# Performance work log

Hardware: AMD Instinct MI355X
Metric: run time of the kernel (lower is better)

The kernel has to match this reference:

```python
import jax, jax.numpy as jnp
import numpy as np

D_MODEL = 1024
D_FF = 4096
FFN_H = int(2 * D_FF / 3)  # 2730, per SwiGLUMLP
B, S = 4, 4096
LN_EPS = 1e-5
ATTN_EPS = 1e-6


def layer_norm(x, g, b):
    mu = jnp.mean(x, axis=-1, keepdims=True)
    var = jnp.mean(jnp.square(x - mu), axis=-1, keepdims=True)
    return (x - mu) * jax.lax.rsqrt(var + LN_EPS) * g + b


def setup_inputs() -> dict:
    key = jax.random.key(0)
    ks = jax.random.split(key, 16)
    s = 0.02
    return {
        "x": jax.random.normal(ks[0], (B, S, D_MODEL), dtype=jnp.float32),
        "Wqkv": jax.random.normal(ks[1], (D_MODEL, 3 * D_MODEL), dtype=jnp.float32) * s,
        "bqkv": jnp.zeros((3 * D_MODEL,), jnp.float32),
        "Wg": jax.random.normal(ks[2], (D_MODEL, FFN_H), dtype=jnp.float32) * s,
        "bg": jnp.zeros((FFN_H,), jnp.float32),
        "Wu": jax.random.normal(ks[3], (D_MODEL, FFN_H), dtype=jnp.float32) * s,
        "bu": jnp.zeros((FFN_H,), jnp.float32),
        "Wd": jax.random.normal(ks[4], (FFN_H, D_MODEL), dtype=jnp.float32) * s,
        "bd": jnp.zeros((D_MODEL,), jnp.float32),
        "g1": jnp.ones((D_MODEL,), jnp.float32),
        "b1": jnp.zeros((D_MODEL,), jnp.float32),
        "g2": jnp.ones((D_MODEL,), jnp.float32),
        "b2": jnp.zeros((D_MODEL,), jnp.float32),
    }


def reference(x, Wqkv, bqkv, Wg, bg, Wu, bu, Wd, bd, g1, b1, g2, b2):
    # QKV projection, split into q, k, v (each [B,S,D])
    qkv = jnp.einsum("bsd,de->bse", x, Wqkv) + bqkv
    q, k, v = jnp.split(qkv, 3, axis=-1)

    # Linear attention with elu(x)+1 feature map (non-causal)
    qp = jax.nn.elu(q) + 1.0
    kp = jax.nn.elu(k) + 1.0
    kv = jnp.einsum("bsd,bse->bde", kp, v)        # [B,D,D] context
    num = jnp.einsum("bsd,bde->bse", qp, kv)       # [B,S,D]
    k_sum = jnp.sum(kp, axis=1)                    # [B,D]
    den = jnp.einsum("bsd,bd->bs", qp, k_sum)[..., None]
    attn = num / (den + ATTN_EPS)

    x = layer_norm(x + attn, g1, b1)

    # SwiGLU MLP
    gate = jnp.einsum("bsd,dh->bsh", x, Wg) + bg
    up = jnp.einsum("bsd,dh->bsh", x, Wu) + bu
    ffn = jnp.einsum("bsh,hd->bsd", jax.nn.silu(gate) * up, Wd) + bd

    return layer_norm(x + ffn, g2, b2)
```

## Files before the change

kernel.cpp:

```cpp
#include <hip/hip_runtime.h>

#define SEQ 4096
#define TOK 16384
#define DM 1024
#define NQKV 3072
#define FFH 2730
#define FFHP 2816

typedef __bf16 bf16x8 __attribute__((ext_vector_type(8)));
typedef float f32x4 __attribute__((ext_vector_type(4)));

__device__ __forceinline__ unsigned short f2bf(float f) {
  union { float f; unsigned u; } v; v.f = f;
  unsigned r = v.u + 0x7fffu + ((v.u >> 16) & 1u);
  return (unsigned short)(r >> 16);
}
__device__ __forceinline__ float bf2f(unsigned short h) {
  union { unsigned u; float f; } v; v.u = ((unsigned)h) << 16;
  return v.f;
}

__device__ __forceinline__ void xcd_swizzle(int& bx, int& by) {
  const int gx = gridDim.x, gy = gridDim.y;
  const int chunk = gy >> 3;
  const int csh = __ffs(chunk) - 1;
  const int lin = by * gx + bx;
  const int xcd = lin & 7, j = lin >> 3;
  by = xcd * chunk + (j & (chunk - 1));
  bx = j >> csh;
}

enum { M_QKV = 0, M_BF16 = 1, M_NUM = 2, M_BIAS_F32 = 5 };

template<int MODE>
__global__ __launch_bounds__(256)
void gemm_kernel(const unsigned short* __restrict__ A,
                 const unsigned short* __restrict__ BT,
                 int K, int lda, int ldb, int ldc,
                 long zsA, long zsB, long zsC,
                 void* __restrict__ out0, void* __restrict__ out1, void* __restrict__ out2,
                 const float* __restrict__ bias, int nbias)
{
  __shared__ unsigned short As[2][128 * 64];
  __shared__ unsigned short Bs[2][128 * 64];
  const int tid  = threadIdx.x;
  const int wave = tid >> 6, lane = tid & 63;
  const int quad = lane >> 4, l16 = lane & 15;
  const int bz = blockIdx.z;
  int bx = blockIdx.x, by = blockIdx.y;
  xcd_swizzle(bx, by);

  const unsigned short* Ab = A + (size_t)zsA * bz + (size_t)by * 128 * lda;
  const unsigned short* Bb = BT + (size_t)zsB * bz + (size_t)bx * 128 * ldb;

  f32x4 acc[4][4] = {};

  const int srow   = lane >> 3;
  const int scol_g = (((lane & 7) ^ srow) * 8);
  const int axor   = l16 & 7;

  auto stage = [&](int buf, int k0) {
#pragma unroll
    for (int j = 0; j < 4; ++j) {
      int c = wave * 4 + j;
      const unsigned short* sa = Ab + (size_t)(c * 8 + srow) * lda + k0 + scol_g;
      __builtin_amdgcn_global_load_lds((__attribute__((address_space(1))) void*)sa,
          (__attribute__((address_space(3))) void*)(As[buf] + c * 512), 16, 0, 0);
      const unsigned short* sb = Bb + (size_t)(c * 8 + srow) * ldb + k0 + scol_g;
      __builtin_amdgcn_global_load_lds((__attribute__((address_space(1))) void*)sb,
          (__attribute__((address_space(3))) void*)(Bs[buf] + c * 512), 16, 0, 0);
    }
  };

  const int NIT = K >> 6;
  stage(0, 0);
  int cur = 0;
  for (int it = 0; it < NIT; ++it) {
    __builtin_amdgcn_s_waitcnt(0);
    __syncthreads();
    if (it + 1 < NIT) stage(cur ^ 1, (it + 1) << 6);
#pragma unroll
    for (int kk = 0; kk < 64; kk += 32) {
      bf16x8 af[4], bfr[4];
#pragma unroll
      for (int mt = 0; mt < 4; ++mt)
        af[mt] = *(const bf16x8*)(As[cur] + ((wave >> 1) * 64 + mt * 16 + l16) * 64
                                     + ((((kk >> 3) + quad) ^ axor) * 8));
#pragma unroll
      for (int nt = 0; nt < 4; ++nt)
        bfr[nt] = *(const bf16x8*)(Bs[cur] + ((wave & 1) * 64 + nt * 16 + l16) * 64
                                      + ((((kk >> 3) + quad) ^ axor) * 8));
#pragma unroll
      for (int mt = 0; mt < 4; ++mt)
#pragma unroll
        for (int nt = 0; nt < 4; ++nt)
          acc[mt][nt] = __builtin_amdgcn_mfma_f32_16x16x32_bf16(af[mt], bfr[nt], acc[mt][nt], 0, 0, 0);
    }
    cur ^= 1;
  }

#pragma unroll
  for (int mt = 0; mt < 4; ++mt) {
#pragma unroll
    for (int nt = 0; nt < 4; ++nt) {
      const int r0 = by * 128 + (wave >> 1) * 64 + mt * 16 + quad * 4;
      const int c  = bx * 128 + (wave & 1) * 64 + nt * 16 + l16;
      float vals[4];
#pragma unroll
      for (int i = 0; i < 4; ++i) vals[i] = acc[mt][nt][i];

      if (MODE == M_QKV) {
        const int b = r0 >> 12, s0 = r0 & 4095;
#pragma unroll
        for (int i = 0; i < 4; ++i) vals[i] += bias[c];
        if (c < 1024) {
#pragma unroll
          for (int i = 0; i < 4; ++i) {
            float e = vals[i] > 0.f ? vals[i] + 1.f : __expf(vals[i]);
            ((unsigned short*)out0)[(size_t)(r0 + i) * DM + c] = f2bf(e);
          }
        } else if (c < 2048) {
          ushort4 o;
          float e0 = vals[0] > 0.f ? vals[0] + 1.f : __expf(vals[0]);
          float e1 = vals[1] > 0.f ? vals[1] + 1.f : __expf(vals[1]);
          float e2 = vals[2] > 0.f ? vals[2] + 1.f : __expf(vals[2]);
          float e3 = vals[3] > 0.f ? vals[3] + 1.f : __expf(vals[3]);
          o.x = f2bf(e0); o.y = f2bf(e1); o.z = f2bf(e2); o.w = f2bf(e3);
          *(ushort4*)((unsigned short*)out1 + (size_t)b * DM * SEQ + (size_t)(c - 1024) * SEQ + s0) = o;
        } else {
          ushort4 o;
          o.x = f2bf(vals[0]); o.y = f2bf(vals[1]); o.z = f2bf(vals[2]); o.w = f2bf(vals[3]);
          *(ushort4*)((unsigned short*)out2 + (size_t)b * DM * SEQ + (size_t)(c - 2048) * SEQ + s0) = o;
        }
      } else {
#pragma unroll
        for (int i = 0; i < 4; ++i) {
          const int r = r0 + i;
          float val = vals[i];
          if (MODE == M_BF16 || MODE == M_NUM) {
            ((unsigned short*)out0)[(size_t)zsC * bz + (size_t)r * ldc + c] = f2bf(val);
          } else {
            if (c < nbias) val += bias[c];
            ((float*)out0)[(size_t)r * ldc + c] = val;
          }
        }
      }
    }
  }
}

enum { G_GATEUP = 0, G_NUM = 1, G_BIAS_F32 = 2 };

#define MBAR() asm volatile("s_barrier" ::: "memory")
#define WAITV(N) asm volatile("s_waitcnt vmcnt(" #N ")" ::: "memory")

#define LDS_A(BUF, QM) do {                                                   \
    _Pragma("unroll")                                                         \
    for (int mt = 0; mt < 4; ++mt) {                                          \
      _Pragma("unroll")                                                       \
      for (int k2 = 0; k2 < 2; ++k2)                                          \
        af[mt][k2] = *(const bf16x8*)(As[BUF] +                               \
            (wm * 128 + ((QM) * 4 + mt) * 16 + l16) * 64 +                    \
            (((k2 * 4 + quad) ^ axor) * 8));                                  \
    }                                                                         \
  } while (0)

#define LDS_B(BUF, QN) do {                                                   \
    _Pragma("unroll")                                                         \
    for (int nt = 0; nt < 2; ++nt) {                                          \
      _Pragma("unroll")                                                       \
      for (int k2 = 0; k2 < 2; ++k2)                                          \
        bfr[nt][k2] = *(const bf16x8*)(Bs[BUF] +                              \
            (wn * 64 + ((QN) * 2 + nt) * 16 + l16) * 64 +                     \
            (((k2 * 4 + quad) ^ axor) * 8));                                  \
    }                                                                         \
  } while (0)

#define MMAQ(QM, QN) do {                                                     \
    _Pragma("unroll")                                                         \
    for (int mt = 0; mt < 4; ++mt) {                                          \
      _Pragma("unroll")                                                       \
      for (int nt = 0; nt < 2; ++nt) {                                        \
        _Pragma("unroll")                                                     \
        for (int k2 = 0; k2 < 2; ++k2)                                        \
          acc[(QM) * 4 + mt][(QN) * 2 + nt] =                                 \
              __builtin_amdgcn_mfma_f32_16x16x32_bf16(af[mt][k2], bfr[nt][k2],\
                  acc[(QM) * 4 + mt][(QN) * 2 + nt], 0, 0, 0);                \
      }                                                                       \
    }                                                                         \
  } while (0)

#define PHASE(BUF, QM, QN, LA, LB, STAGE) do {                                \
    if (LA) LDS_A(BUF, QM);                                                   \
    if (LB) LDS_B(BUF, QN);                                                   \
    STAGE                                                                     \
    MBAR();                                                                   \
    __builtin_amdgcn_sched_barrier(0);                                        \
    __builtin_amdgcn_s_setprio(1);                                            \
    MMAQ(QM, QN);                                                             \
    __builtin_amdgcn_s_setprio(0);                                            \
    WAITV(6);                                                                 \
    MBAR();                                                                   \
  } while (0)

template<int MODE>
__global__ __launch_bounds__(512, 2)
void gemm256_kernel(const unsigned short* __restrict__ A,
                    const unsigned short* __restrict__ BT,
                    int K, int lda, int ldb, int ldc,
                    long zsA, long zsB, long zsC,
                    void* __restrict__ out0,
                    const float* __restrict__ bias0,
                    const float* __restrict__ bias1,
                    int nbias)
{
  __shared__ unsigned short As[2][256 * 64];
  __shared__ unsigned short Bs[2][256 * 64];
  const int tid  = threadIdx.x;
  const int wave = tid >> 6, lane = tid & 63;
  const int quad = lane >> 4, l16 = lane & 15;
  const int wm = wave >> 2, wn = wave & 3;
  const int bz = blockIdx.z;
  int bx = blockIdx.x, by = blockIdx.y;
  xcd_swizzle(bx, by);

  const unsigned short* Ab = A + (size_t)zsA * bz + (size_t)by * 256 * lda;
  const unsigned short* Bb = BT + (size_t)zsB * bz + (size_t)bx * 256 * ldb;

  f32x4 acc[8][4] = {};

  const int srow = lane >> 3;
  const int sxor = ((lane & 7) ^ srow) * 8;
  const int axor = l16 & 7;

  const unsigned short* pA[2][2];
  const unsigned short* pB[2][2];
  int cA[2][2], cB[2][2];
#pragma unroll
  for (int part = 0; part < 2; ++part) {
#pragma unroll
    for (int j = 0; j < 2; ++j) {
      int idx = wave * 2 + j;
      int ca = ((idx & 8) ? idx + 8 : idx) + part * 8;
      int cb = (idx >> 2) * 8 + (idx & 3) + part * 4;
      cA[part][j] = ca; cB[part][j] = cb;
      pA[part][j] = Ab + (size_t)(ca * 8 + srow) * lda + sxor;
      pB[part][j] = Bb + (size_t)(cb * 8 + srow) * ldb + sxor;
    }
  }

  auto stageA = [&](int buf, int part, int tile) {
    const int k0 = tile << 6;
#pragma unroll
    for (int j = 0; j < 2; ++j)
      __builtin_amdgcn_global_load_lds(
          (__attribute__((address_space(1))) void*)(pA[part][j] + k0),
          (__attribute__((address_space(3))) void*)(As[buf] + cA[part][j] * 512), 16, 0, 0);
  };
  auto stageB = [&](int buf, int part, int tile) {
    const int k0 = tile << 6;
#pragma unroll
    for (int j = 0; j < 2; ++j)
      __builtin_amdgcn_global_load_lds(
          (__attribute__((address_space(1))) void*)(pB[part][j] + k0),
          (__attribute__((address_space(3))) void*)(Bs[buf] + cB[part][j] * 512), 16, 0, 0);
  };

  stageA(0, 0, 0); stageA(0, 1, 0); stageB(0, 0, 0); stageB(0, 1, 0);
  stageB(1, 0, 1); stageA(1, 1, 1);
  WAITV(4);
  MBAR();

  bf16x8 af[4][2], bfr[2][2];
  const int NT = K >> 6;
  for (int i = 0; i < NT; i += 2) {
    const int t1 = i + 1;
    const int t2s = (i + 2 < NT), t3s = (i + 3 < NT);
    PHASE(0, 0, 0, 1, 1, { stageA(1, 0, t1); });
    PHASE(0, 1, 0, 1, 0, { stageB(1, 1, t1); });
    PHASE(0, 1, 1, 0, 1, { if (t2s) stageB(0, 0, i + 2); });
    PHASE(0, 0, 1, 1, 0, { if (t2s) stageA(0, 1, i + 2); });
    PHASE(1, 0, 0, 1, 1, { if (t2s) stageA(0, 0, i + 2); });
    PHASE(1, 1, 0, 1, 0, { if (t2s) stageB(0, 1, i + 2); });
    PHASE(1, 1, 1, 0, 1, { if (t3s) stageB(1, 0, i + 3); });
    PHASE(1, 0, 1, 1, 0, { if (t3s) stageA(1, 1, i + 3); });
  }

  if (MODE == G_GATEUP) {
#pragma unroll
    for (int mt = 0; mt < 8; ++mt) {
      const int r0 = by * 256 + wm * 128 + mt * 16 + quad * 4;
#pragma unroll
      for (int p = 0; p < 2; ++p) {
        const int hc = bx * 128 + wn * 32 + p * 16 + l16;
        const float bgv = (hc < nbias) ? bias0[hc] : 0.f;
        const float buv = (hc < nbias) ? bias1[hc] : 0.f;
#pragma unroll
        for (int i2 = 0; i2 < 4; ++i2) {
          float g = acc[mt][2 * p][i2] + bgv;
          float u = acc[mt][2 * p + 1][i2] + buv;
          float hv = g / (1.f + __expf(-g)) * u;
          ((unsigned short*)out0)[(size_t)(r0 + i2) * ldc + hc] = f2bf(hv);
        }
      }
    }
  } else {
#pragma unroll
    for (int mt = 0; mt < 8; ++mt) {
#pragma unroll
      for (int nt = 0; nt < 4; ++nt) {
        const int r0 = by * 256 + wm * 128 + mt * 16 + quad * 4;
        const int c  = bx * 256 + wn * 64 + nt * 16 + l16;
#pragma unroll
        for (int i2 = 0; i2 < 4; ++i2) {
          float v = acc[mt][nt][i2];
          if (MODE == G_NUM) {
            ((unsigned short*)out0)[(size_t)zsC * bz + (size_t)(r0 + i2) * ldc + c] = f2bf(v);
          } else {
            if (c < nbias) v += bias0[c];
            ((float*)out0)[(size_t)(r0 + i2) * ldc + c] = v;
          }
        }
      }
    }
  }
}

__global__ __launch_bounds__(256)
void cvt_kernel(const float* __restrict__ in, unsigned short* __restrict__ out, int n)
{
  int i = (blockIdx.x * 256 + threadIdx.x) * 4;
  if (i < n) {
    float4 v = *(const float4*)(in + i);
    ushort4 o;
    o.x = f2bf(v.x); o.y = f2bf(v.y); o.z = f2bf(v.z); o.w = f2bf(v.w);
    *(ushort4*)(out + i) = o;
  }
}

__global__ __launch_bounds__(256)
void wtrans_kernel(const float* __restrict__ in, unsigned short* __restrict__ out,
                   int R, int C, int Cpad, int Rpad, int omode)
{
  __shared__ float tile[32][33];
  int r0 = blockIdx.x * 32;
  int c0 = blockIdx.y * 32;
  int tid = threadIdx.x;
#pragma unroll
  for (int j = 0; j < 4; ++j) {
    int r = j * 8 + (tid >> 5), c = tid & 31;
    float v = 0.f;
    if (r0 + r < R && c0 + c < C) v = in[(size_t)(r0 + r) * C + c0 + c];
    tile[r][c] = v;
  }
  __syncthreads();
#pragma unroll
  for (int j = 0; j < 4; ++j) {
    int c = j * 8 + (tid >> 5), r = tid & 31;
    int oc = c0 + c;
    int orow = (omode == 0) ? oc
             : ((oc >> 4) * 32 + (oc & 15) + ((omode == 2) ? 16 : 0));
    out[(size_t)orow * Rpad + (r0 + r)] = f2bf(tile[r][c]);
  }
}

__device__ __forceinline__ float block_sum(float v, float* sm)
{
#pragma unroll
  for (int o = 32; o > 0; o >>= 1) v += __shfl_down(v, o, 64);
  int w = threadIdx.x >> 6;
  if ((threadIdx.x & 63) == 0) sm[w] = v;
  __syncthreads();
  float r = sm[0] + sm[1] + sm[2] + sm[3];
  __syncthreads();
  return r;
}

__global__ __launch_bounds__(256)
void ksum_kernel(const unsigned short* __restrict__ kpT, float* __restrict__ ksum)
{
  __shared__ float sm[4];
  int row = blockIdx.x;
  const ushort4* src = (const ushort4*)(kpT + (size_t)row * SEQ);
  float s = 0.f;
#pragma unroll
  for (int j = 0; j < 4; ++j) {
    ushort4 v = src[threadIdx.x + j * 256];
    s += bf2f(v.x) + bf2f(v.y) + bf2f(v.z) + bf2f(v.w);
  }
  float tot = block_sum(s, sm);
  if (threadIdx.x == 0) ksum[row] = tot;
}

__global__ __launch_bounds__(256)
void ln1_kernel(const unsigned short* __restrict__ xb16, const unsigned short* __restrict__ num16,
                const unsigned short* __restrict__ qp, const float* __restrict__ ksum,
                const float* __restrict__ g1, const float* __restrict__ b1,
                unsigned short* __restrict__ yb)
{
  __shared__ float sm[4];
  int t = blockIdx.x, tid = threadIdx.x, b = t >> 12;
  ushort4 xv = ((const ushort4*)(xb16 + (size_t)t * DM))[tid];
  ushort4 nv = ((const ushort4*)(num16 + (size_t)t * DM))[tid];
  ushort4 qv = ((const ushort4*)(qp + (size_t)t * DM))[tid];
  float4 kv = ((const float4*)(ksum + (size_t)b * DM))[tid];
  float q0 = bf2f(qv.x), q1 = bf2f(qv.y), q2 = bf2f(qv.z), q3 = bf2f(qv.w);
  float den = block_sum(q0 * kv.x + q1 * kv.y + q2 * kv.z + q3 * kv.w, sm);
  float inv = 1.f / (den + 1e-6f);
  float r0 = bf2f(xv.x) + bf2f(nv.x) * inv, r1 = bf2f(xv.y) + bf2f(nv.y) * inv;
  float r2 = bf2f(xv.z) + bf2f(nv.z) * inv, r3 = bf2f(xv.w) + bf2f(nv.w) * inv;
  float s1 = block_sum(r0 + r1 + r2 + r3, sm);
  float s2 = block_sum(r0 * r0 + r1 * r1 + r2 * r2 + r3 * r3, sm);
  float mu = s1 * (1.f / 1024.f);
  float var = s2 * (1.f / 1024.f) - mu * mu;
  float rs = rsqrtf(var + 1e-5f);
  float4 gv = ((const float4*)g1)[tid];
  float4 bv = ((const float4*)b1)[tid];
  ushort4 o;
  o.x = f2bf((r0 - mu) * rs * gv.x + bv.x);
  o.y = f2bf((r1 - mu) * rs * gv.y + bv.y);
  o.z = f2bf((r2 - mu) * rs * gv.z + bv.z);
  o.w = f2bf((r3 - mu) * rs * gv.w + bv.w);
  ((ushort4*)(yb + (size_t)t * DM))[tid] = o;
}

__global__ __launch_bounds__(256)
void ln2_kernel(const unsigned short* __restrict__ yb, const float* __restrict__ ffn,
                const float* __restrict__ g2, const float* __restrict__ b2,
                float* __restrict__ out)
{
  __shared__ float sm[4];
  int t = blockIdx.x, tid = threadIdx.x;
  ushort4 yv = ((const ushort4*)(yb + (size_t)t * DM))[tid];
  float4 fv = ((const float4*)(ffn + (size_t)t * DM))[tid];
  float r0 = bf2f(yv.x) + fv.x, r1 = bf2f(yv.y) + fv.y;
  float r2 = bf2f(yv.z) + fv.z, r3 = bf2f(yv.w) + fv.w;
  float s1 = block_sum(r0 + r1 + r2 + r3, sm);
  float s2 = block_sum(r0 * r0 + r1 * r1 + r2 * r2 + r3 * r3, sm);
  float mu = s1 * (1.f / 1024.f);
  float var = s2 * (1.f / 1024.f) - mu * mu;
  float rs = rsqrtf(var + 1e-5f);
  float4 gv = ((const float4*)g2)[tid];
  float4 bv = ((const float4*)b2)[tid];
  float4 o;
  o.x = (r0 - mu) * rs * gv.x + bv.x;
  o.y = (r1 - mu) * rs * gv.y + bv.y;
  o.z = (r2 - mu) * rs * gv.z + bv.z;
  o.w = (r3 - mu) * rs * gv.w + bv.w;
  ((float4*)(out + (size_t)t * DM))[tid] = o;
}

extern "C" void kernel_launch(void* const* d_in, const int* in_sizes, int n_in,
                              void* d_out, int out_size, void* d_ws, size_t ws_size,
                              hipStream_t stream)
{
  const float* x    = (const float*)d_in[0];
  const float* Wqkv = (const float*)d_in[1];
  const float* bqkv = (const float*)d_in[2];
  const float* Wg   = (const float*)d_in[3];
  const float* bg   = (const float*)d_in[4];
  const float* Wu   = (const float*)d_in[5];
  const float* bu   = (const float*)d_in[6];
  const float* Wd   = (const float*)d_in[7];
  const float* bd   = (const float*)d_in[8];
  const float* g1   = (const float*)d_in[9];
  const float* b1   = (const float*)d_in[10];
  const float* g2   = (const float*)d_in[11];
  const float* b2   = (const float*)d_in[12];
  float* out = (float*)d_out;

  char* ws = (char*)d_ws;
  size_t off = 0;
  auto alloc = [&](size_t bytes) {
    char* p = ws + off;
    off += (bytes + 255) & ~(size_t)255;
    return p;
  };
  unsigned short* WqkvT = (unsigned short*)alloc((size_t)NQKV * DM * 2);
  unsigned short* WguT  = (unsigned short*)alloc((size_t)2 * FFHP * DM * 2);
  unsigned short* WdT   = (unsigned short*)alloc((size_t)DM * FFHP * 2);
  float*          ksum  = (float*)alloc((size_t)4 * DM * 4);
  unsigned short* xbyb  = (unsigned short*)alloc((size_t)TOK * DM * 2);
  unsigned short* kvT   = (unsigned short*)alloc((size_t)4 * DM * DM * 2);
  char* R3 = alloc((size_t)3 * TOK * DM * 2);
  unsigned short* qp  = (unsigned short*)(R3);
  unsigned short* kpT = (unsigned short*)(R3 + (size_t)TOK * DM * 2);
  unsigned short* vT  = (unsigned short*)(R3 + (size_t)2 * TOK * DM * 2);
  unsigned short* hbuf = (unsigned short*)(R3);
  unsigned short* xb = xbyb;
  unsigned short* yb = xbyb;
  unsigned short* num = (unsigned short*)d_out;
  float* ffn = (float*)d_out;

  dim3 blk(256), blk5(512);

  cvt_kernel<<<dim3(TOK * DM / 1024), blk, 0, stream>>>(x, xb, TOK * DM);
  wtrans_kernel<<<dim3(32, 96), blk, 0, stream>>>(Wqkv, WqkvT, 1024, 3072, 3072, 1024, 0);
  wtrans_kernel<<<dim3(32, 88), blk, 0, stream>>>(Wg, WguT, 1024, FFH, FFHP, 1024, 1);
  wtrans_kernel<<<dim3(32, 88), blk, 0, stream>>>(Wu, WguT, 1024, FFH, FFHP, 1024, 2);
  wtrans_kernel<<<dim3(88, 32), blk, 0, stream>>>(Wd, WdT, FFH, 1024, 1024, FFHP, 0);
  gemm_kernel<M_QKV><<<dim3(NQKV / 128, TOK / 128), blk, 0, stream>>>(
      xb, WqkvT, 1024, 1024, 1024, 0, 0, 0, 0, qp, kpT, vT, bqkv, NQKV);
  ksum_kernel<<<dim3(4096), blk, 0, stream>>>(kpT, ksum);
  gemm_kernel<M_BF16><<<dim3(8, 8, 4), blk, 0, stream>>>(
      vT, kpT, 4096, 4096, 4096, 1024,
      (long)DM * SEQ, (long)DM * SEQ, (long)DM * DM,
      kvT, nullptr, nullptr, nullptr, 0);
  gemm256_kernel<G_NUM><<<dim3(4, 16, 4), blk5, 0, stream>>>(
      qp, kvT, 1024, 1024, 1024, 1024,
      (long)SEQ * DM, (long)DM * DM, (long)SEQ * DM,
      num, nullptr, nullptr, 0);
  ln1_kernel<<<dim3(TOK), blk, 0, stream>>>(xb, num, qp, ksum, g1, b1, yb);
  gemm256_kernel<G_GATEUP><<<dim3(2 * FFHP / 256, TOK / 256), blk5, 0, stream>>>(
      yb, WguT, 1024, DM, DM, FFHP, 0, 0, 0, hbuf, bg, bu, FFH);
  gemm256_kernel<G_BIAS_F32><<<dim3(DM / 256, TOK / 256), blk5, 0, stream>>>(
      hbuf, WdT, FFHP, FFHP, FFHP, DM, 0, 0, 0, ffn, bd, nullptr, DM);
  ln2_kernel<<<dim3(TOK), blk, 0, stream>>>(yb, ffn, g2, b2, out);

  (void)in_sizes; (void)n_in; (void)out_size; (void)ws_size;
}
```

Baseline: 786.6 us.

## Restructure 256-tile GEMM LDS schedule and move QKV projection onto it

The 256x256 GEMM now loads all A and B fragments for a k-tile from LDS at once, into double register sets, before its four MFMA phases, and reorders the global-to-LDS prefetch stages to match. The QKV projection moves from the 128-tile gemm_kernel to this 256-tile kernel with a new epilogue that applies the elu+1 feature map and writes q, the transposed k and the transposed v. The aim is fewer LDS-read stalls between phases and a more efficient large-tile kernel for QKV. In exchange it raises register pressure, which may hurt occupancy at launch bounds of 512 threads and 2 blocks, and the QKV epilogue uses scalar bias loads with a per-column branch.

```diff
diff --git a/kernel.cpp b/kernel.cpp
--- a/kernel.cpp
+++ b/kernel.cpp
@@ -149,29 +149,40 @@
   }
 }
 
-enum { G_GATEUP = 0, G_NUM = 1, G_BIAS_F32 = 2 };
+enum { G_GATEUP = 0, G_NUM = 1, G_BIAS_F32 = 2, G_QKV = 3 };
 
 #define MBAR() asm volatile("s_barrier" ::: "memory")
 #define WAITV(N) asm volatile("s_waitcnt vmcnt(" #N ")" ::: "memory")
 
-#define LDS_A(BUF, QM) do {                                                   \
+#define LDS_ALL(BUF) do {                                                     \
     _Pragma("unroll")                                                         \
     for (int mt = 0; mt < 4; ++mt) {                                          \
       _Pragma("unroll")                                                       \
       for (int k2 = 0; k2 < 2; ++k2)                                          \
-        af[mt][k2] = *(const bf16x8*)(As[BUF] +                               \
-            (wm * 128 + ((QM) * 4 + mt) * 16 + l16) * 64 +                    \
-            (((k2 * 4 + quad) ^ axor) * 8));                                  \
+        af[0][mt][k2] = *(const bf16x8*)(As[BUF] +                            \
+            (wm * 128 + mt * 16 + l16) * 64 + (((k2 * 4 + quad) ^ axor) * 8));\
     }                                                                         \
-  } while (0)
-
-#define LDS_B(BUF, QN) do {                                                   \
     _Pragma("unroll")                                                         \
     for (int nt = 0; nt < 2; ++nt) {                                          \
       _Pragma("unroll")                                                       \
       for (int k2 = 0; k2 < 2; ++k2)                                          \
-        bfr[nt][k2] = *(const bf16x8*)(Bs[BUF] +                              \
-            (wn * 64 + ((QN) * 2 + nt) * 16 + l16) * 64 +                     \
+        bfr[0][nt][k2] = *(const bf16x8*)(Bs[BUF] +                           \
+            (wn * 64 + nt * 16 + l16) * 64 + (((k2 * 4 + quad) ^ axor) * 8)); \
+    }                                                                         \
+    _Pragma("unroll")                                                         \
+    for (int mt = 0; mt < 4; ++mt) {                                          \
+      _Pragma("unroll")                                                       \
+      for (int k2 = 0; k2 < 2; ++k2)                                          \
+        af[1][mt][k2] = *(const bf16x8*)(As[BUF] +                            \
+            (wm * 128 + (4 + mt) * 16 + l16) * 64 +                           \
+            (((k2 * 4 + quad) ^ axor) * 8));                                  \
+    }                                                                         \
+    _Pragma("unroll")                                                         \
+    for (int nt = 0; nt < 2; ++nt) {                                          \
+      _Pragma("unroll")                                                       \
+      for (int k2 = 0; k2 < 2; ++k2)                                          \
+        bfr[1][nt][k2] = *(const bf16x8*)(Bs[BUF] +                           \
+            (wn * 64 + (2 + nt) * 16 + l16) * 64 +                            \
             (((k2 * 4 + quad) ^ axor) * 8));                                  \
     }                                                                         \
   } while (0)
@@ -184,15 +195,13 @@
         _Pragma("unroll")                                                     \
         for (int k2 = 0; k2 < 2; ++k2)                                        \
           acc[(QM) * 4 + mt][(QN) * 2 + nt] =                                 \
-              __builtin_amdgcn_mfma_f32_16x16x32_bf16(af[mt][k2], bfr[nt][k2],\
-                  acc[(QM) * 4 + mt][(QN) * 2 + nt], 0, 0, 0);                \
+              __builtin_amdgcn_mfma_f32_16x16x32_bf16(af[QM][mt][k2],         \
+                  bfr[QN][nt][k2], acc[(QM) * 4 + mt][(QN) * 2 + nt], 0, 0, 0);\
       }                                                                       \
     }                                                                         \
   } while (0)
 
-#define PHASE(BUF, QM, QN, LA, LB, STAGE) do {                                \
-    if (LA) LDS_A(BUF, QM);                                                   \
-    if (LB) LDS_B(BUF, QN);                                                   \
+#define PHASE(QM, QN, STAGE) do {                                             \
     STAGE                                                                     \
     MBAR();                                                                   \
     __builtin_amdgcn_sched_barrier(0);                                        \
@@ -210,6 +219,7 @@
                     int K, int lda, int ldb, int ldc,
                     long zsA, long zsB, long zsC,
                     void* __restrict__ out0,
+                    void* __restrict__ out1, void* __restrict__ out2,
                     const float* __restrict__ bias0,
                     const float* __restrict__ bias1,
                     int nbias)
@@ -266,24 +276,25 @@
           (__attribute__((address_space(3))) void*)(Bs[buf] + cB[part][j] * 512), 16, 0, 0);
   };
 
-  stageA(0, 0, 0); stageA(0, 1, 0); stageB(0, 0, 0); stageB(0, 1, 0);
-  stageB(1, 0, 1); stageA(1, 1, 1);
-  WAITV(4);
+  stageA(0, 0, 0); stageB(0, 0, 0); stageA(0, 1, 0); stageB(0, 1, 0);
+  stageA(1, 0, 1); stageB(1, 0, 1); stageA(1, 1, 1);
+  WAITV(6);
   MBAR();
 
-  bf16x8 af[4][2], bfr[2][2];
+  bf16x8 af[2][4][2], bfr[2][2][2];
   const int NT = K >> 6;
   for (int i = 0; i < NT; i += 2) {
-    const int t1 = i + 1;
     const int t2s = (i + 2 < NT), t3s = (i + 3 < NT);
-    PHASE(0, 0, 0, 1, 1, { stageA(1, 0, t1); });
-    PHASE(0, 1, 0, 1, 0, { stageB(1, 1, t1); });
-    PHASE(0, 1, 1, 0, 1, { if (t2s) stageB(0, 0, i + 2); });
-    PHASE(0, 0, 1, 1, 0, { if (t2s) stageA(0, 1, i + 2); });
-    PHASE(1, 0, 0, 1, 1, { if (t2s) stageA(0, 0, i + 2); });
-    PHASE(1, 1, 0, 1, 0, { if (t2s) stageB(0, 1, i + 2); });
-    PHASE(1, 1, 1, 0, 1, { if (t3s) stageB(1, 0, i + 3); });
-    PHASE(1, 0, 1, 1, 0, { if (t3s) stageA(1, 1, i + 3); });
+    LDS_ALL(0);
+    PHASE(0, 0, { stageB(1, 1, i + 1); });
+    PHASE(1, 0, { if (t2s) stageA(0, 0, i + 2); });
+    PHASE(1, 1, { if (t2s) stageB(0, 0, i + 2); });
+    PHASE(0, 1, { if (t2s) stageA(0, 1, i + 2); });
+    LDS_ALL(1);
+    PHASE(0, 0, { if (t2s) stageB(0, 1, i + 2); });
+    PHASE(1, 0, { if (t3s) stageA(1, 0, i + 3); });
+    PHASE(1, 1, { if (t3s) stageB(1, 0, i + 3); });
+    PHASE(0, 1, { if (t3s) stageA(1, 1, i + 3); });
   }
 
   if (MODE == G_GATEUP) {
@@ -301,6 +312,38 @@
           float u = acc[mt][2 * p + 1][i2] + buv;
           float hv = g / (1.f + __expf(-g)) * u;
           ((unsigned short*)out0)[(size_t)(r0 + i2) * ldc + hc] = f2bf(hv);
+        }
+      }
+    }
+  } else if (MODE == G_QKV) {
+#pragma unroll
+    for (int mt = 0; mt < 8; ++mt) {
+#pragma unroll
+      for (int nt = 0; nt < 4; ++nt) {
+        const int r0 = by * 256 + wm * 128 + mt * 16 + quad * 4;
+        const int c  = bx * 256 + wn * 64 + nt * 16 + l16;
+        const int b = r0 >> 12, s0 = r0 & 4095;
+        float vals[4];
+#pragma unroll
+        for (int i2 = 0; i2 < 4; ++i2) vals[i2] = acc[mt][nt][i2] + bias0[c];
+        if (c < 1024) {
+#pragma unroll
+          for (int i2 = 0; i2 < 4; ++i2) {
+            float e = vals[i2] > 0.f ? vals[i2] + 1.f : __expf(vals[i2]);
+            ((unsigned short*)out0)[(size_t)(r0 + i2) * DM + c] = f2bf(e);
+          }
+        } else if (c < 2048) {
+          ushort4 o;
+          float e0 = vals[0] > 0.f ? vals[0] + 1.f : __expf(vals[0]);
+          float e1 = vals[1] > 0.f ? vals[1] + 1.f : __expf(vals[1]);
+          float e2 = vals[2] > 0.f ? vals[2] + 1.f : __expf(vals[2]);
+          float e3 = vals[3] > 0.f ? vals[3] + 1.f : __expf(vals[3]);
+          o.x = f2bf(e0); o.y = f2bf(e1); o.z = f2bf(e2); o.w = f2bf(e3);
+          *(ushort4*)((unsigned short*)out1 + (size_t)b * DM * SEQ + (size_t)(c - 1024) * SEQ + s0) = o;
+        } else {
+          ushort4 o;
+          o.x = f2bf(vals[0]); o.y = f2bf(vals[1]); o.z = f2bf(vals[2]); o.w = f2bf(vals[3]);
+          *(ushort4*)((unsigned short*)out2 + (size_t)b * DM * SEQ + (size_t)(c - 2048) * SEQ + s0) = o;
         }
       }
     }
@@ -499,8 +542,8 @@
   wtrans_kernel<<<dim3(32, 88), blk, 0, stream>>>(Wg, WguT, 1024, FFH, FFHP, 1024, 1);
   wtrans_kernel<<<dim3(32, 88), blk, 0, stream>>>(Wu, WguT, 1024, FFH, FFHP, 1024, 2);
   wtrans_kernel<<<dim3(88, 32), blk, 0, stream>>>(Wd, WdT, FFH, 1024, 1024, FFHP, 0);
-  gemm_kernel<M_QKV><<<dim3(NQKV / 128, TOK / 128), blk, 0, stream>>>(
-      xb, WqkvT, 1024, 1024, 1024, 0, 0, 0, 0, qp, kpT, vT, bqkv, NQKV);
+  gemm256_kernel<G_QKV><<<dim3(NQKV / 256, TOK / 256), blk5, 0, stream>>>(
+      xb, WqkvT, 1024, 1024, 1024, 0, 0, 0, 0, qp, kpT, vT, bqkv, nullptr, NQKV);
   ksum_kernel<<<dim3(4096), blk, 0, stream>>>(kpT, ksum);
   gemm_kernel<M_BF16><<<dim3(8, 8, 4), blk, 0, stream>>>(
       vT, kpT, 4096, 4096, 4096, 1024,
@@ -509,12 +552,12 @@
   gemm256_kernel<G_NUM><<<dim3(4, 16, 4), blk5, 0, stream>>>(
       qp, kvT, 1024, 1024, 1024, 1024,
       (long)SEQ * DM, (long)DM * DM, (long)SEQ * DM,
-      num, nullptr, nullptr, 0);
+      num, nullptr, nullptr, nullptr, nullptr, 0);
   ln1_kernel<<<dim3(TOK), blk, 0, stream>>>(xb, num, qp, ksum, g1, b1, yb);
   gemm256_kernel<G_GATEUP><<<dim3(2 * FFHP / 256, TOK / 256), blk5, 0, stream>>>(
-      yb, WguT, 1024, DM, DM, FFHP, 0, 0, 0, hbuf, bg, bu, FFH);
+      yb, WguT, 1024, DM, DM, FFHP, 0, 0, 0, hbuf, nullptr, nullptr, bg, bu, FFH);
   gemm256_kernel<G_BIAS_F32><<<dim3(DM / 256, TOK / 256), blk5, 0, stream>>>(
-      hbuf, WdT, FFHP, FFHP, FFHP, DM, 0, 0, 0, ffn, bd, nullptr, DM);
+      hbuf, WdT, FFHP, FFHP, FFHP, DM, 0, 0, 0, ffn, nullptr, nullptr, bd, nullptr, DM);
   ln2_kernel<<<dim3(TOK), blk, 0, stream>>>(yb, ffn, g2, b2, out);
 
   (void)in_sizes; (void)n_in; (void)out_size; (void)ws_size;
```

Result: slower. 838.5 us (+6.6%).
